# Optimization experiments

Hardware: AMD Instinct MI355X
Metric: run time of the kernel (lower is better)

## Reference

```python
import jax, jax.numpy as jnp
import numpy as np

B, N, D = 4, 2048, 256
EPS = 1e-5


def _clinear(Z, W, b):
    # complex linear: Z (B,2,N,din), W (2,dout,din), b (2,dout)
    Zr, Zi = Z[:, 0], Z[:, 1]
    Wr, Wi = W[0], W[1]
    outr = Zr @ Wr.T - Zi @ Wi.T + b[0]
    outi = Zr @ Wi.T + Zi @ Wr.T + b[1]
    return jnp.stack([outr, outi], axis=1)


def setup_inputs() -> dict:
    key = jax.random.key(0)
    ks = jax.random.split(key, 14)
    sc = 1.0 / np.sqrt(D).astype(np.float32)
    t = jnp.tile(jnp.arange(N + 1, dtype=jnp.float32)[None] * 0.01, (B, 1))
    return {
        'Z_q': jax.random.normal(ks[0], (B, 2, N, D), jnp.float32),
        'Z_k': jax.random.normal(ks[1], (B, 2, N, D), jnp.float32),
        'Z_v': jax.random.normal(ks[2], (B, 2, N, D), jnp.float32),
        't_measure_all': t,
        'W_q': jax.random.normal(ks[3], (2, D, D), jnp.float32) * sc,
        'b_q': jax.random.normal(ks[4], (2, D), jnp.float32) * 0.01,
        'W_k': jax.random.normal(ks[5], (2, D, D), jnp.float32) * sc,
        'b_k': jax.random.normal(ks[6], (2, D), jnp.float32) * 0.01,
        'W_v': jax.random.normal(ks[7], (2, D, D), jnp.float32) * sc,
        'b_v': jax.random.normal(ks[8], (2, D), jnp.float32) * 0.01,
        'W_p': jax.random.normal(ks[9], (2, D, D), jnp.float32) * sc,
        'b_p': jax.random.normal(ks[10], (2, D), jnp.float32) * 0.01,
        'lambda1': jax.random.normal(ks[11], (2, D // 2, 1), jnp.float32),
        'lambda_Omega_sqrt': jax.random.normal(ks[12], (1, D, 1), jnp.float32) * sc,
        'lambda_Gamma_sqrt': jax.random.normal(ks[13], (1, D, 1), jnp.float32) * sc,
        'tau': jnp.asarray(1.0, jnp.float32),
        'delta': jnp.asarray(0.0, jnp.float32),
        'lambda_C': jnp.ones((1, D, 1), jnp.float32),
    }


def reference(Z_q, Z_k, Z_v, t_measure_all, W_q, b_q, W_k, b_k, W_v, b_v,
              W_p, b_p, lambda1, lambda_Omega_sqrt, lambda_Gamma_sqrt,
              tau, delta, lambda_C):
    # lambda_h = 0 * compute_lambda_h(lambda1): conjugate-pair spectrum, zeroed in forward
    lam_r = 0.0 * jnp.concatenate([lambda1[0], lambda1[0]], axis=0)[:, 0]   # (D,)
    lam_i = 0.0 * jnp.concatenate([lambda1[1], -lambda1[1]], axis=0)[:, 0]  # (D,)
    lam_Om = lambda_Omega_sqrt ** 2 + EPS   # process noise (1,D,1)
    lam_Ga = lambda_Gamma_sqrt ** 2 + EPS   # measurement noise (1,D,1)

    Q = _clinear(Z_q, W_q, b_q)  # (B,2,N,D)
    K = _clinear(Z_k, W_k, b_k)
    V = _clinear(Z_v, W_v, b_v)

    t = t_measure_all[0, :-1]  # (N,)
    # exponential state-transition kernels exp(+/- lambda * t): (2,N,D)
    mag_f = jnp.exp(lam_r[None] * t[:, None]); ph_f = lam_i[None] * t[:, None]
    exp_f = jnp.stack([mag_f * jnp.cos(ph_f), mag_f * jnp.sin(ph_f)])
    mag_b = jnp.exp(-lam_r[None] * t[:, None]); ph_b = -lam_i[None] * t[:, None]
    exp_b = jnp.stack([mag_b * jnp.cos(ph_b), mag_b * jnp.sin(ph_b)])
    # one-step transition exp(lambda * dt): (2,D)
    dt = t[1] - t[0]
    mat_exp = jnp.stack([jnp.exp(lam_r * dt) * jnp.cos(lam_i * dt),
                         jnp.exp(lam_r * dt) * jnp.sin(lam_i * dt)])

    # averaged covariance kernel, exact lambda->0 limit: Gamma + Omega*|t_i-t_j|, mean over D
    lamC2 = lambda_C[0, :, 0] ** 2
    ga_bar = jnp.mean(lamC2 * lam_Ga[0, :, 0])
    om_bar = jnp.mean(lamC2 * lam_Om[0, :, 0])
    abs_dt = jnp.abs(t[:, None] - t[None, :])          # (N,N)
    V_avg_ij = ga_bar + om_bar * abs_dt                # (N,N)

    # factorized kernels
    V_v = exp_f[None]                 # (1,2,N,D)
    U_q = exp_b[None] * Q             # (B,2,N,D)
    U_k = exp_b[None] * K
    U_v = exp_b[None] * V

    # precision-weighted squared residual norm R_ij = sum_d |V_k|^2 |U_q_i - U_k_j|^2
    Vk_abs = jnp.sum(exp_f ** 2, axis=0)              # (N,D)
    Uk_abs = jnp.sum(U_k ** 2, axis=1)                # (B,N,D)
    Uq_abs = jnp.sum(U_q ** 2, axis=1)                # (B,N,D)
    T1 = jnp.einsum('id,bjd->bij', Vk_abs, Uk_abs)
    T2 = jnp.sum(Vk_abs[None] * Uq_abs, axis=2)[:, :, None]
    T3 = (jnp.einsum('bid,bjd->bij', Vk_abs[None] * U_q[:, 0], U_k[:, 0]) +
          jnp.einsum('bid,bjd->bij', Vk_abs[None] * U_q[:, 1], U_k[:, 1]))
    R_qk_abs = T1 + T2 - 2.0 * T3                     # (B,N,N)

    scores = -(tau ** 2) * jnp.log(V_avg_ij[None] + R_qk_abs)
    mask = jnp.tril(jnp.ones((N, N), bool))
    scores = jnp.where(mask[None], scores, -jnp.inf)
    A = jax.nn.softmax(scores, axis=2)                # (B,N,N)
    Q_ij = jnp.stack([A, jnp.zeros_like(A)], axis=1)  # (B,2,N,N)

    # est_inner = complex matmul(Q_ij, U_v); Q imag part is zero
    est_inner = jnp.stack([jnp.einsum('bij,bjd->bid', A, U_v[:, 0]),
                           jnp.einsum('bij,bjd->bid', A, U_v[:, 1])], axis=1)
    est_v = V_v * est_inner          # plain elementwise product, as in source
    s = jax.nn.sigmoid(delta)
    est_eigenbasis = (1.0 - s) * V + s * est_v        # (B,2,N,D)

    # complex Hadamard with one-step transition
    pr = mat_exp[0][None, None] * est_eigenbasis[:, 0] - mat_exp[1][None, None] * est_eigenbasis[:, 1]
    pi = mat_exp[0][None, None] * est_eigenbasis[:, 1] + mat_exp[1][None, None] * est_eigenbasis[:, 0]
    pred_p = jnp.stack([pr, pi], axis=1)
    out = _clinear(pred_p, W_p, b_p)                  # (B,2,N,D)

    lambda_h = jnp.stack([lam_r, lam_i])[..., None]
    return est_eigenbasis, out, Q_ij, V_v, U_v, lambda_h
```

## Files before the change

### kernel.cpp

```cpp
#include <hip/hip_runtime.h>
#include <math.h>

#define BN 4
#define NN 2048
#define DD 256
#define EPSF 1e-5f

typedef __attribute__((ext_vector_type(8))) short bf16x8;
typedef __attribute__((ext_vector_type(4))) float f32x4;

constexpr size_t OFF_EST = 0;
constexpr size_t OFF_OUT = (size_t)BN * 2 * NN * DD;
constexpr size_t OFF_QIJ = OFF_OUT + (size_t)BN * 2 * NN * DD;
constexpr size_t OFF_VV  = OFF_QIJ + (size_t)BN * 2 * NN * NN;
constexpr size_t OFF_UV  = OFF_VV + (size_t)2 * NN * DD;
constexpr size_t OFF_LH  = OFF_UV + (size_t)BN * 2 * NN * DD;

constexpr size_t SCR_B0   = OFF_QIJ + (size_t)NN * NN;
constexpr size_t U_Q16    = 0;
constexpr size_t U_K16    = (size_t)BN * NN * DD;
constexpr size_t U_VT16   = 2 * (size_t)BN * NN * DD;
constexpr size_t SCR_QN   = SCR_B0 + 3 * (size_t)BN * NN * DD / 2;
constexpr size_t SCR_KN   = SCR_QN + (size_t)BN * NN;
constexpr size_t SCR_L    = SCR_KN + (size_t)BN * NN;
constexpr size_t SCR_SC   = SCR_L + (size_t)BN * NN;
constexpr size_t SCR_W16P = SCR_SC + 16;
constexpr size_t SCR_E16F = OFF_QIJ + 3 * (size_t)NN * NN;
constexpr size_t U_PART   = (size_t)BN * NN * 512;
constexpr size_t SCR_Z16F = OFF_QIJ + 5 * (size_t)NN * NN;
constexpr size_t SCR_Z16VF = OFF_QIJ + 7 * (size_t)NN * NN;
constexpr size_t U_W16    = (size_t)BN * NN * 512;

constexpr size_t W16_PER_B = 136 * 16384;

__device__ __forceinline__ short f2bf(float x) {
    union { float f; unsigned u; } v; v.f = x;
    unsigned r = v.u + 0x7fff + ((v.u >> 16) & 1);
    return (short)(r >> 16);
}
__device__ __forceinline__ float bf2f(unsigned short h) {
    union { unsigned u; float f; } v; v.u = ((unsigned)h) << 16;
    return v.f;
}
__device__ __forceinline__ unsigned short* u16p(float* d, size_t fofs) {
    return (unsigned short*)(d + fofs);
}
__device__ __forceinline__ const unsigned short* u16pc(const float* d, size_t fofs) {
    return (const unsigned short*)(d + fofs);
}
__device__ __forceinline__ unsigned short* w16p(float* d, int b) {
    return (b < 3) ? u16p(d, SCR_Z16F) + (size_t)b * W16_PER_B
                   : u16p(d, SCR_Z16VF);
}
__device__ __forceinline__ const unsigned short* w16pc(const float* d, int b) {
    return (b < 3) ? u16pc(d, SCR_Z16F) + (size_t)b * W16_PER_B
                   : u16pc(d, SCR_Z16VF);
}
__device__ __forceinline__ int nc_of(int TI) { return TI >= 12 ? 3 : (TI >= 6 ? 2 : 1); }
__device__ __forceinline__ int cb_of(int TI) {
    return TI < 6 ? TI : (TI < 12 ? 6 + 2 * (TI - 6) : 18 + 3 * (TI - 12));
}

__device__ __forceinline__ void gll16(const unsigned short* g, short* l) {
    __builtin_amdgcn_global_load_lds(
        (const __attribute__((address_space(1))) unsigned*)g,
        (__attribute__((address_space(3))) unsigned*)l, 16, 0, 0);
}
__device__ __forceinline__ void stage_tile(const unsigned short* gbase, size_t stride_sh,
                                           short* ldsbuf, int t) {
    const int w = t >> 6, L = t & 63;
#pragma unroll
    for (int p = 0; p < 2; ++p) {
        const int r0 = w * 32 + p * 16;
        const unsigned short* src = gbase + (size_t)(r0 + (L >> 2)) * stride_sh + (L & 3) * 8;
        gll16(src, ldsbuf + r0 * 32);
    }
}

__global__ void k_cvt(const float* __restrict__ Zq, const float* __restrict__ Zk,
                      const float* __restrict__ Zv,
                      const float* __restrict__ Wq, const float* __restrict__ Wk,
                      const float* __restrict__ Wv, const float* __restrict__ Wp,
                      const float* __restrict__ tau, const float* __restrict__ delta,
                      const float* __restrict__ lamOm, const float* __restrict__ lamGa,
                      const float* __restrict__ lamC,
                      float* __restrict__ dout) {
    const int z = blockIdx.z;
    if (z < 3) {
        const float* Z = (z == 0) ? Zq : (z == 1) ? Zk : Zv;
        unsigned short* O = (z == 0) ? u16p(dout, SCR_Z16F)
                          : (z == 1) ? u16p(dout, SCR_Z16F) + (size_t)BN * NN * 512
                                     : u16p(dout, SCR_Z16VF);
        const long n4 = (long)BN * 2 * NN * DD / 4;
        for (long i4 = (long)blockIdx.x * 256 + threadIdx.x; i4 < n4;
             i4 += (long)gridDim.x * 256) {
            const long i = i4 * 4;
            const int d = (int)(i & (DD - 1));
            const long r = i >> 8;
            const int n = (int)(r & (NN - 1));
            const long bc = r >> 11;
            const int c = (int)(bc & 1), b = (int)(bc >> 1);
            float4 v = *(const float4*)&Z[i];
            ushort4 o;
            o.x = (unsigned short)f2bf(v.x); o.y = (unsigned short)f2bf(v.y);
            o.z = (unsigned short)f2bf(v.z); o.w = (unsigned short)f2bf(v.w);
            *(ushort4*)&O[((size_t)(b * NN + n)) * 512 + c * 256 + d] = o;
        }
    } else if (z == 3) {
        const float* Ws[4] = {Wq, Wk, Wv, Wp};
        const long n4 = 6L * 256 * 512 / 4;
        for (long e4 = (long)blockIdx.x * 256 + threadIdx.x; e4 < n4;
             e4 += (long)gridDim.x * 256) {
            const long e = e4 * 4;
            const int k = (int)(e & 511);
            const long rest = e >> 9;
            const int dd = (int)(rest & 255);
            const int m = (int)(rest >> 8);
            int proj, mode;
            if (m < 3)      { proj = m; mode = 0; }
            else if (m == 3){ proj = 2; mode = 1; }
            else            { proj = 3; mode = m - 4; }
            const int kc = k >> 8, kk = k & 255;
            int wc; float sgn;
            if (mode == 0) { wc = kc; sgn = kc ? -1.f : 1.f; }
            else           { wc = 1 - kc; sgn = 1.f; }
            float4 v = *(const float4*)&Ws[proj][((size_t)wc * DD + dd) * DD + kk];
            ushort4 o;
            o.x = (unsigned short)f2bf(sgn * v.x); o.y = (unsigned short)f2bf(sgn * v.y);
            o.z = (unsigned short)f2bf(sgn * v.z); o.w = (unsigned short)f2bf(sgn * v.w);
            unsigned short* dst = (m < 4)
                ? u16p(dout, SCR_Z16VF) + U_W16 + (size_t)m * 131072
                : u16p(dout, SCR_W16P) + (size_t)(m - 4) * 131072;
            *(ushort4*)&dst[(size_t)dd * 512 + k] = o;
        }
    } else {
        const int idx = blockIdx.x * 256 + threadIdx.x;
        if (idx < 3 * BN * NN) dout[SCR_QN + idx] = 0.f;
        if (blockIdx.x == 0) {
            __shared__ float red[8];
            const int t = threadIdx.x;
            float c2 = lamC[t] * lamC[t];
            float ga = c2 * (lamGa[t] * lamGa[t] + EPSF);
            float om = c2 * (lamOm[t] * lamOm[t] + EPSF);
            for (int o = 32; o > 0; o >>= 1) {
                ga += __shfl_down(ga, o, 64);
                om += __shfl_down(om, o, 64);
            }
            if ((t & 63) == 0) { red[t >> 6] = ga; red[4 + (t >> 6)] = om; }
            __syncthreads();
            if (t == 0) {
                float gs = red[0] + red[1] + red[2] + red[3];
                float os = red[4] + red[5] + red[6] + red[7];
                float* scal = dout + SCR_SC;
                scal[0] = tau[0] * tau[0];
                scal[1] = 1.f / (1.f + __expf(-delta[0]));
                scal[2] = gs / 256.f;
                scal[3] = os / 256.f;
            }
        }
    }
}

__global__ __launch_bounds__(256) void k_qkv(const float* __restrict__ bq,
                                             const float* __restrict__ bk,
                                             const float* __restrict__ bv,
                                             float* __restrict__ dout)
{
    __shared__ short Al[128 * 32];
    __shared__ short Bl[128 * 32];
    const int z = blockIdx.z;
    const int d0 = blockIdx.x * 128;
    const int b = blockIdx.y >> 4;
    const int n0 = (blockIdx.y & 15) * 128;

    const unsigned short* Z16 =
        (z == 0) ? u16pc(dout, SCR_Z16F)
      : (z == 1) ? u16pc(dout, SCR_Z16F) + (size_t)BN * NN * 512
                 : u16pc(dout, SCR_Z16VF);
    const unsigned short* W16 = u16pc(dout, SCR_Z16VF) + U_W16 + (size_t)z * 131072;
    const float* bias = (z == 0) ? bq : (z == 1) ? bk : bv;
    const int bofs = (z == 3) ? DD : 0;

    const int t = threadIdx.x, wave = t >> 6, lane = t & 63, quad = lane >> 4, lm = lane & 15;
    const int wm = (wave >> 1) * 64, wn = (wave & 1) * 64;
    const unsigned short* Abase = Z16 + (size_t)(b * NN + n0) * 512;
    const unsigned short* Bbase = W16 + (size_t)d0 * 512;

    f32x4 acc[4][4];
#pragma unroll
    for (int i = 0; i < 4; ++i)
#pragma unroll
        for (int j = 0; j < 4; ++j) acc[i][j] = (f32x4){0.f, 0.f, 0.f, 0.f};

    for (int kt = 0; kt < 16; ++kt) {
        const int kk0 = kt * 32;
        stage_tile(Abase + kk0, 512, Al, t);
        stage_tile(Bbase + kk0, 512, Bl, t);
        __syncthreads();
        bf16x8 af[4], bff[4];
#pragma unroll
        for (int mi = 0; mi < 4; ++mi) af[mi] = *(const bf16x8*)&Al[(wm + mi * 16 + lm) * 32 + quad * 8];
#pragma unroll
        for (int nj = 0; nj < 4; ++nj) bff[nj] = *(const bf16x8*)&Bl[(wn + nj * 16 + lm) * 32 + quad * 8];
#pragma unroll
        for (int mi = 0; mi < 4; ++mi)
#pragma unroll
            for (int nj = 0; nj < 4; ++nj)
                acc[mi][nj] = __builtin_amdgcn_mfma_f32_16x16x32_bf16(af[mi], bff[nj], acc[mi][nj], 0, 0, 0);
        __syncthreads();
    }

    if (z <= 1) {
        unsigned short* O16 = u16p(dout, SCR_B0) + (z ? U_K16 : U_Q16) + (size_t)b * NN * DD;
        float* NRM = dout + (z ? SCR_KN : SCR_QN) + b * NN;
#pragma unroll
        for (int mi = 0; mi < 4; ++mi)
#pragma unroll
            for (int r = 0; r < 4; ++r) {
                const int m = n0 + wm + mi * 16 + quad * 4 + r;
                float ss = 0.f;
#pragma unroll
                for (int nj = 0; nj < 4; ++nj) {
                    const int d = d0 + wn + nj * 16 + lm;
                    unsigned short h = (unsigned short)f2bf(acc[mi][nj][r] + bias[d]);
                    O16[(size_t)m * DD + d] = h;
                    const float vb = bf2f(h);
                    ss = fmaf(vb, vb, ss);
                }
                ss += __shfl_down(ss, 8, 16); ss += __shfl_down(ss, 4, 16);
                ss += __shfl_down(ss, 2, 16); ss += __shfl_down(ss, 1, 16);
                if (lm == 0) atomicAdd(&NRM[m], ss);
            }
    } else if (z == 2) {
        float* UV0 = dout + OFF_UV + (size_t)(b * 2) * NN * DD;
#pragma unroll
        for (int mi = 0; mi < 4; ++mi)
#pragma unroll
            for (int r = 0; r < 4; ++r) {
                const int m = n0 + wm + mi * 16 + quad * 4 + r;
#pragma unroll
                for (int nj = 0; nj < 4; ++nj) {
                    const int d = d0 + wn + nj * 16 + lm;
                    UV0[(size_t)m * DD + d] = acc[mi][nj][r] + bias[d];
                }
            }
    } else {
        const float s1 = 1.f - dout[SCR_SC + 1];
        float* EST1 = dout + OFF_EST + (size_t)(b * 2 + 1) * NN * DD;
        unsigned short* E16 = u16p(dout, SCR_E16F) + (size_t)b * NN * 512;
#pragma unroll
        for (int mi = 0; mi < 4; ++mi)
#pragma unroll
            for (int r = 0; r < 4; ++r) {
                const int m = n0 + wm + mi * 16 + quad * 4 + r;
#pragma unroll
                for (int nj = 0; nj < 4; ++nj) {
                    const int d = d0 + wn + nj * 16 + lm;
                    const float v = s1 * (acc[mi][nj][r] + bias[bofs + d]);
                    EST1[(size_t)m * DD + d] = v;
                    E16[(size_t)m * 512 + 256 + d] = (unsigned short)f2bf(v);
                }
            }
    }
}

__global__ __launch_bounds__(256) void k_outproj(const float* __restrict__ bp,
                                                 float* __restrict__ dout)
{
    __shared__ short Al[128 * 32];
    __shared__ short Bl[128 * 32];
    const int z = blockIdx.z;
    const int d0 = blockIdx.x * 128;
    const int b = blockIdx.y >> 4;
    const int n0 = (blockIdx.y & 15) * 128;
    const unsigned short* E16 = u16pc(dout, SCR_E16F) + (size_t)b * NN * 512;
    const unsigned short* W16 = u16pc(dout, SCR_W16P) + (size_t)z * 131072;

    const int t = threadIdx.x, wave = t >> 6, lane = t & 63, quad = lane >> 4, lm = lane & 15;
    const int wm = (wave >> 1) * 64, wn = (wave & 1) * 64;
    const unsigned short* Abase = E16 + (size_t)n0 * 512;
    const unsigned short* Bbase = W16 + (size_t)d0 * 512;

    f32x4 acc[4][4];
#pragma unroll
    for (int i = 0; i < 4; ++i)
#pragma unroll
        for (int j = 0; j < 4; ++j) acc[i][j] = (f32x4){0.f, 0.f, 0.f, 0.f};

    for (int kt = 0; kt < 16; ++kt) {
        const int kk0 = kt * 32;
        stage_tile(Abase + kk0, 512, Al, t);
        stage_tile(Bbase + kk0, 512, Bl, t);
        __syncthreads();
        bf16x8 af[4], bff[4];
#pragma unroll
        for (int mi = 0; mi < 4; ++mi) af[mi] = *(const bf16x8*)&Al[(wm + mi * 16 + lm) * 32 + quad * 8];
#pragma unroll
        for (int nj = 0; nj < 4; ++nj) bff[nj] = *(const bf16x8*)&Bl[(wn + nj * 16 + lm) * 32 + quad * 8];
#pragma unroll
        for (int mi = 0; mi < 4; ++mi)
#pragma unroll
            for (int nj = 0; nj < 4; ++nj)
                acc[mi][nj] = __builtin_amdgcn_mfma_f32_16x16x32_bf16(af[mi], bff[nj], acc[mi][nj], 0, 0, 0);
        __syncthreads();
    }
    const int bofs = z ? DD : 0;
    float* O = dout + OFF_OUT + (size_t)(b * 2 + z) * NN * DD;
#pragma unroll
    for (int mi = 0; mi < 4; ++mi)
#pragma unroll
        for (int r = 0; r < 4; ++r) {
            const int m = n0 + wm + mi * 16 + quad * 4 + r;
#pragma unroll
            for (int nj = 0; nj < 4; ++nj) {
                const int d = d0 + wn + nj * 16 + lm;
                O[(size_t)m * DD + d] = acc[mi][nj][r] + bp[bofs + d];
            }
        }
}

__global__ void k_vtrans(float* __restrict__ dout) {
    __shared__ float T[64][65];
    const int b = blockIdx.z;
    const int nb = blockIdx.x * 64, db = blockIdx.y * 64;
    const float* V = dout + OFF_UV + (size_t)(b * 2) * NN * DD;
    unsigned short* VT = u16p(dout, SCR_B0) + U_VT16 + (size_t)b * DD * NN;
    const int tr = threadIdx.x >> 4, tc = (threadIdx.x & 15) * 4;
#pragma unroll
    for (int p = 0; p < 4; ++p) {
        float4 v = *(const float4*)&V[(size_t)(nb + tr + p * 16) * DD + db + tc];
        T[tr + p * 16][tc + 0] = v.x; T[tr + p * 16][tc + 1] = v.y;
        T[tr + p * 16][tc + 2] = v.z; T[tr + p * 16][tc + 3] = v.w;
    }
    __syncthreads();
#pragma unroll
    for (int p = 0; p < 4; ++p) {
        const int d = tr + p * 16;
        ushort4 o;
        o.x = (unsigned short)f2bf(T[tc + 0][d]);
        o.y = (unsigned short)f2bf(T[tc + 1][d]);
        o.z = (unsigned short)f2bf(T[tc + 2][d]);
        o.w = (unsigned short)f2bf(T[tc + 3][d]);
        *(ushort4*)&VT[(size_t)(db + d) * NN + nb + tc] = o;
    }
}

__global__ __launch_bounds__(256) void k_scores(const float* __restrict__ tmeas,
                                                float* __restrict__ dout) {
    __shared__ short Al[128 * 32];
    __shared__ short Bl[128 * 32];
    const int b = blockIdx.y, x = blockIdx.x;
    int ti = (int)((sqrtf(8.f * x + 1.f) - 1.f) * 0.5f);
    while ((ti + 1) * (ti + 2) / 2 <= x) ++ti;
    while (ti * (ti + 1) / 2 > x) --ti;
    const int tj = x - ti * (ti + 1) / 2;
    const int i0 = ti * 128, j0 = tj * 128;
    const unsigned short* Q16 = u16pc(dout, SCR_B0) + U_Q16 + (size_t)b * NN * DD;
    const unsigned short* K16 = u16pc(dout, SCR_B0) + U_K16 + (size_t)b * NN * DD;
    const int t = threadIdx.x, wave = t >> 6, lane = t & 63, quad = lane >> 4, lm = lane & 15;
    const int wm = (wave >> 1) * 64, wn = (wave & 1) * 64;
    const unsigned short* Abase = Q16 + (size_t)i0 * DD;
    const unsigned short* Bbase = K16 + (size_t)j0 * DD;

    f32x4 acc[4][4];
#pragma unroll
    for (int i = 0; i < 4; ++i)
#pragma unroll
        for (int j = 0; j < 4; ++j) acc[i][j] = (f32x4){0.f, 0.f, 0.f, 0.f};

    for (int kt = 0; kt < 8; ++kt) {
        const int kk0 = kt * 32;
        stage_tile(Abase + kk0, DD, Al, t);
        stage_tile(Bbase + kk0, DD, Bl, t);
        __syncthreads();
        bf16x8 af[4], bff[4];
#pragma unroll
        for (int mi = 0; mi < 4; ++mi) af[mi] = *(const bf16x8*)&Al[(wm + mi * 16 + lm) * 32 + quad * 8];
#pragma unroll
        for (int nj = 0; nj < 4; ++nj) bff[nj] = *(const bf16x8*)&Bl[(wn + nj * 16 + lm) * 32 + quad * 8];
#pragma unroll
        for (int mi = 0; mi < 4; ++mi)
#pragma unroll
            for (int nj = 0; nj < 4; ++nj)
                acc[mi][nj] = __builtin_amdgcn_mfma_f32_16x16x32_bf16(af[mi], bff[nj], acc[mi][nj], 0, 0, 0);
        __syncthreads();
    }

    const float tau2 = dout[SCR_SC + 0], ga = dout[SCR_SC + 2], om = dout[SCR_SC + 3];
    unsigned short* WT = w16p(dout, b) + (size_t)x * 16384;
    const float* QN_ = dout + SCR_QN + b * NN;
    const float* KN_ = dout + SCR_KN + b * NN;
    float kn[4], tjv[4]; int jj[4];
#pragma unroll
    for (int nj = 0; nj < 4; ++nj) {
        jj[nj] = j0 + wn + nj * 16 + lm;
        kn[nj] = KN_[jj[nj]];
        tjv[nj] = tmeas[jj[nj]];
    }
#pragma unroll
    for (int mi = 0; mi < 4; ++mi)
#pragma unroll
        for (int r = 0; r < 4; ++r) {
            const int li = wm + mi * 16 + quad * 4 + r;
            const int i = i0 + li;
            const float qni = QN_[i], tqi = tmeas[i];
            float rs = 0.f;
#pragma unroll
            for (int nj = 0; nj < 4; ++nj) {
                float xx = ga + om * fabsf(tqi - tjv[nj]) + qni + kn[nj] - 2.f * acc[mi][nj][r];
                xx = fmaxf(xx, 1e-30f);
                float w = (tau2 == 1.f) ? __builtin_amdgcn_rcpf(xx)
                                        : __expf(-tau2 * __logf(xx));
                if (jj[nj] > i) w = 0.f;
                const unsigned short h = (unsigned short)f2bf(w);
                WT[(size_t)li * 128 + (wn + nj * 16 + lm)] = h;
                rs += bf2f(h);
            }
            rs += __shfl_down(rs, 8, 16); rs += __shfl_down(rs, 4, 16);
            rs += __shfl_down(rs, 2, 16); rs += __shfl_down(rs, 1, 16);
            if (lm == 0) atomicAdd(&dout[SCR_L + b * NN + i], rs);
        }
}

__global__ __launch_bounds__(256) void k_estinner(float* __restrict__ dout) {
    __shared__ short Al[128 * 32];
    __shared__ short Bl[128 * 32];
    const int b = blockIdx.y;
    const int chunk = blockIdx.x >> 1, half = blockIdx.x & 1;
    int y = chunk, TI = 0, cb = 0;
    for (;;) { const int nc = nc_of(TI); if (y < nc) break; y -= nc; cb += nc; ++TI; }
    const int kbeg = y * 768;
    const int kend = min(kbeg + 768, (TI + 1) * 128);
    const int nst = (kend - kbeg) >> 5;
    const int cidx = cb + y;
    const int tri = TI * (TI + 1) / 2;
    const unsigned short* WT = w16pc(dout, b);
    const unsigned short* VT = u16pc(dout, SCR_B0) + U_VT16 + (size_t)b * DD * NN
                             + (size_t)(half * 128) * NN;

    const int t = threadIdx.x, wave = t >> 6, lane = t & 63, quad = lane >> 4, lm = lane & 15;
    const int wm = (wave >> 1) * 64, wn = (wave & 1) * 64;

    f32x4 acc[4][4];
#pragma unroll
    for (int i = 0; i < 4; ++i)
#pragma unroll
        for (int j = 0; j < 4; ++j) acc[i][j] = (f32x4){0.f, 0.f, 0.f, 0.f};

    for (int kt = 0; kt < nst; ++kt) {
        const int kk0 = kbeg + kt * 32;
        const int tile = kk0 >> 7;
        stage_tile(WT + (size_t)(tri + tile) * 16384 + (kk0 & 127), 128, Al, t);
        stage_tile(VT + kk0, NN, Bl, t);
        __syncthreads();
        bf16x8 af[4], bff[4];
#pragma unroll
        for (int mi = 0; mi < 4; ++mi) af[mi] = *(const bf16x8*)&Al[(wm + mi * 16 + lm) * 32 + quad * 8];
#pragma unroll
        for (int nj = 0; nj < 4; ++nj) bff[nj] = *(const bf16x8*)&Bl[(wn + nj * 16 + lm) * 32 + quad * 8];
#pragma unroll
        for (int mi = 0; mi < 4; ++mi)
#pragma unroll
            for (int nj = 0; nj < 4; ++nj)
                acc[mi][nj] = __builtin_amdgcn_mfma_f32_16x16x32_bf16(af[mi], bff[nj], acc[mi][nj], 0, 0, 0);
        __syncthreads();
    }
    unsigned short* P = u16p(dout, SCR_E16F) + U_PART +
                        ((size_t)(b * 30 + cidx)) * 128 * 256;
#pragma unroll
    for (int mi = 0; mi < 4; ++mi)
#pragma unroll
        for (int r = 0; r < 4; ++r) {
            const int ri = wm + mi * 16 + quad * 4 + r;
#pragma unroll
            for (int nj = 0; nj < 4; ++nj) {
                const int d = half * 128 + wn + nj * 16 + lm;
                P[(size_t)ri * 256 + d] = (unsigned short)f2bf(acc[mi][nj][r]);
            }
        }
}

__global__ void k_blendfills(float* __restrict__ dout) {
    const int z = blockIdx.z;
    if (z < 4) {
        const int b = z;
        if (blockIdx.x >= 512) return;
        const int t = threadIdx.x;
        const int i = blockIdx.x * 4 + (t >> 6);
        const int d4 = (t & 63) * 4;
        const int TI = i >> 7;
        const int nc = nc_of(TI), cb = cb_of(TI);
        const float s = dout[SCR_SC + 1];
        const float linv = 1.f / dout[SCR_L + b * NN + i];
        const unsigned short* P = u16pc(dout, SCR_E16F) + U_PART;
        float4 sum = {0.f, 0.f, 0.f, 0.f};
        for (int c = 0; c < nc; ++c) {
            ushort4 pv = *(const ushort4*)&P[((size_t)(b * 30 + cb + c) * 128 + (i & 127)) * 256 + d4];
            sum.x += bf2f(pv.x); sum.y += bf2f(pv.y);
            sum.z += bf2f(pv.z); sum.w += bf2f(pv.w);
        }
        const float4 vr = *(const float4*)&dout[OFF_UV + ((size_t)(b * 2) * NN + i) * DD + d4];
        const float sl = s * linv;
        float4 ev;
        ev.x = (1.f - s) * vr.x + sl * sum.x;
        ev.y = (1.f - s) * vr.y + sl * sum.y;
        ev.z = (1.f - s) * vr.z + sl * sum.z;
        ev.w = (1.f - s) * vr.w + sl * sum.w;
        *(float4*)&dout[OFF_EST + ((size_t)(b * 2) * NN + i) * DD + d4] = ev;
        ushort4 o;
        o.x = (unsigned short)f2bf(ev.x); o.y = (unsigned short)f2bf(ev.y);
        o.z = (unsigned short)f2bf(ev.z); o.w = (unsigned short)f2bf(ev.w);
        *(ushort4*)&u16p(dout, SCR_E16F)[((size_t)(b * NN + i)) * 512 + d4] = o;
        return;
    }
    if (z < 8) {
        const int b = z - 4, i = blockIdx.x;
        const int TI = i >> 7, li = i & 127;
        const int tri = TI * (TI + 1) / 2;
        const float linv = 1.f / dout[SCR_L + b * NN + i];
        const unsigned short* WTb = w16pc(dout, b);
        float* row = dout + OFF_QIJ + (size_t)b * 2 * NN * NN + (size_t)i * NN;
        for (int j4 = threadIdx.x * 4; j4 < NN; j4 += 1024) {
            const int tj = j4 >> 7;
            float4 o = {0.f, 0.f, 0.f, 0.f};
            if (tj <= TI) {
                ushort4 h = *(const ushort4*)&WTb[((size_t)(tri + tj)) * 16384
                                                  + (size_t)li * 128 + (j4 & 127)];
                o.x = bf2f(h.x) * linv; o.y = bf2f(h.y) * linv;
                o.z = bf2f(h.z) * linv; o.w = bf2f(h.w) * linv;
            }
            *(float4*)&row[j4] = o;
        }
        return;
    }
    size_t base; long n; float val = 0.f;
    if (z == 8)       { base = SCR_B0; n = 3145728; }
    else if (z == 9)  { base = OFF_VV; n = (long)NN * DD; val = 1.f; }
    else if (z == 10) { base = OFF_VV + (size_t)NN * DD; n = (long)NN * DD; }
    else if (z < 15)  { base = OFF_UV + (size_t)(2 * (z - 11) + 1) * NN * DD; n = (long)NN * DD; }
    else              { base = OFF_LH; n = 512; }
    float* p = dout + base;
    const float4 v = {val, val, val, val};
    for (long i = ((long)blockIdx.x * 256 + threadIdx.x) * 4; i < n;
         i += (long)gridDim.x * 1024)
        *(float4*)&p[i] = v;
}

extern "C" void kernel_launch(void* const* d_in, const int* in_sizes, int n_in,
                              void* d_out, int out_size, void* d_ws, size_t ws_size,
                              hipStream_t stream) {
    const float* Zq = (const float*)d_in[0];
    const float* Zk = (const float*)d_in[1];
    const float* Zv = (const float*)d_in[2];
    const float* tm = (const float*)d_in[3];
    const float* Wq = (const float*)d_in[4];
    const float* bq = (const float*)d_in[5];
    const float* Wk = (const float*)d_in[6];
    const float* bk = (const float*)d_in[7];
    const float* Wv = (const float*)d_in[8];
    const float* bv = (const float*)d_in[9];
    const float* Wp = (const float*)d_in[10];
    const float* bp = (const float*)d_in[11];
    const float* lamOm = (const float*)d_in[13];
    const float* lamGa = (const float*)d_in[14];
    const float* tau = (const float*)d_in[15];
    const float* delta = (const float*)d_in[16];
    const float* lamC = (const float*)d_in[17];
    float* out = (float*)d_out;

    k_cvt<<<dim3(2048, 1, 5), dim3(256), 0, stream>>>(
        Zq, Zk, Zv, Wq, Wk, Wv, Wp, tau, delta, lamOm, lamGa, lamC, out);
    k_qkv<<<dim3(2, 64, 4), dim3(256), 0, stream>>>(bq, bk, bv, out);
    k_vtrans<<<dim3(32, 4, 4), dim3(256), 0, stream>>>(out);
    k_scores<<<dim3(136, 4), dim3(256), 0, stream>>>(tm, out);
    k_estinner<<<dim3(60, 4), dim3(256), 0, stream>>>(out);
    k_blendfills<<<dim3(2048, 1, 16), dim3(256), 0, stream>>>(out);
    k_outproj<<<dim3(2, 64, 2), dim3(256), 0, stream>>>(bp, out);
    hipMemsetAsync((void*)(out + SCR_Z16F),  0, (size_t)NN * NN * 4, stream);
    hipMemsetAsync((void*)(out + SCR_Z16VF), 0, (size_t)NN * NN * 4, stream);
    hipMemsetAsync((void*)(out + SCR_E16F),  0, (size_t)NN * NN * 4, stream);
    hipMemsetAsync((void*)(out + SCR_QN),    0, ((size_t)NN * NN - 3145728) * 4, stream);
}
```

Baseline: 352.2 us.

## Fuse all stages into one persistent kernel with software grid barriers

Replaces seven separate kernel launches with a single persistent kernel of 512 blocks that runs each stage in turn, separated by an atomic-counter grid barrier. The fill work from the old blend kernel moves into the first stage. The aim is to remove per-launch overhead and the tail idle time between dependent kernels. The cost is spin-wait barriers, and correctness depends on all 512 blocks being co-resident; launch_bounds(256,2) is set for that.

New measurement: 1.120 ms. 3.18x slower.

```diff
diff --git a/kernel.cpp b/kernel.cpp
--- a/kernel.cpp
+++ b/kernel.cpp
@@ -30,8 +30,9 @@
 constexpr size_t SCR_Z16F = OFF_QIJ + 5 * (size_t)NN * NN;
 constexpr size_t SCR_Z16VF = OFF_QIJ + 7 * (size_t)NN * NN;
 constexpr size_t U_W16    = (size_t)BN * NN * 512;
-
 constexpr size_t W16_PER_B = 136 * 16384;
+
+#define NBLK 512
 
 __device__ __forceinline__ short f2bf(float x) {
     union { float f; unsigned u; } v; v.f = x;
@@ -61,6 +62,26 @@
     return TI < 6 ? TI : (TI < 12 ? 6 + 2 * (TI - 6) : 18 + 3 * (TI - 12));
 }
 
+__device__ __forceinline__ void gbar(float* dout) {
+    __syncthreads();
+    if (threadIdx.x == 0) {
+        unsigned* cnt = (unsigned*)(dout + SCR_SC + 8);
+        unsigned* gen = cnt + 1;
+        __threadfence();
+        unsigned g = __hip_atomic_load(gen, __ATOMIC_RELAXED, __HIP_MEMORY_SCOPE_AGENT);
+        unsigned a = __hip_atomic_fetch_add(cnt, 1u, __ATOMIC_ACQ_REL, __HIP_MEMORY_SCOPE_AGENT);
+        if (a == (unsigned)NBLK - 1) {
+            __hip_atomic_store(cnt, 0u, __ATOMIC_RELAXED, __HIP_MEMORY_SCOPE_AGENT);
+            __hip_atomic_fetch_add(gen, 1u, __ATOMIC_RELEASE, __HIP_MEMORY_SCOPE_AGENT);
+        } else {
+            while (__hip_atomic_load(gen, __ATOMIC_ACQUIRE, __HIP_MEMORY_SCOPE_AGENT) == g)
+                __builtin_amdgcn_s_sleep(2);
+        }
+        __threadfence();
+    }
+    __syncthreads();
+}
+
 __device__ __forceinline__ void gll16(const unsigned short* g, short* l) {
     __builtin_amdgcn_global_load_lds(
         (const __attribute__((address_space(1))) unsigned*)g,
@@ -77,23 +98,35 @@
     }
 }
 
-__global__ void k_cvt(const float* __restrict__ Zq, const float* __restrict__ Zk,
-                      const float* __restrict__ Zv,
-                      const float* __restrict__ Wq, const float* __restrict__ Wk,
-                      const float* __restrict__ Wv, const float* __restrict__ Wp,
-                      const float* __restrict__ tau, const float* __restrict__ delta,
-                      const float* __restrict__ lamOm, const float* __restrict__ lamGa,
-                      const float* __restrict__ lamC,
-                      float* __restrict__ dout) {
-    const int z = blockIdx.z;
-    if (z < 3) {
-        const float* Z = (z == 0) ? Zq : (z == 1) ? Zk : Zv;
-        unsigned short* O = (z == 0) ? u16p(dout, SCR_Z16F)
-                          : (z == 1) ? u16p(dout, SCR_Z16F) + (size_t)BN * NN * 512
-                                     : u16p(dout, SCR_Z16VF);
-        const long n4 = (long)BN * 2 * NN * DD / 4;
-        for (long i4 = (long)blockIdx.x * 256 + threadIdx.x; i4 < n4;
-             i4 += (long)gridDim.x * 256) {
+__global__ __launch_bounds__(256, 2) void k_mega(
+    const float* __restrict__ Zq, const float* __restrict__ Zk,
+    const float* __restrict__ Zv, const float* __restrict__ tmeas,
+    const float* __restrict__ Wq, const float* __restrict__ bq,
+    const float* __restrict__ Wk, const float* __restrict__ bk,
+    const float* __restrict__ Wv, const float* __restrict__ bv,
+    const float* __restrict__ Wp, const float* __restrict__ bp,
+    const float* __restrict__ lamOm, const float* __restrict__ lamGa,
+    const float* __restrict__ tau, const float* __restrict__ delta,
+    const float* __restrict__ lamC, float* __restrict__ dout)
+{
+    __shared__ __align__(16) float smemf[4160];
+    short* Al = (short*)smemf;
+    short* Bl = ((short*)smemf) + 4096;
+
+    const int t = threadIdx.x;
+    const int wave = t >> 6, lane = t & 63, quad = lane >> 4, lm = lane & 15;
+    const int wm = (wave >> 1) * 64, wn = (wave & 1) * 64;
+
+    {
+        const long tid = (long)blockIdx.x * 256 + t;
+        const long nthr = (long)gridDim.x * 256;
+        for (long u = tid; u < 3L * 1048576; u += nthr) {
+            const int zz = (int)(u >> 20);
+            const long i4 = u & 1048575;
+            const float* Z = (zz == 0) ? Zq : (zz == 1) ? Zk : Zv;
+            unsigned short* O = (zz == 0) ? u16p(dout, SCR_Z16F)
+                              : (zz == 1) ? u16p(dout, SCR_Z16F) + (size_t)BN * NN * 512
+                                          : u16p(dout, SCR_Z16VF);
             const long i = i4 * 4;
             const int d = (int)(i & (DD - 1));
             const long r = i >> 8;
@@ -106,25 +139,22 @@
             o.z = (unsigned short)f2bf(v.z); o.w = (unsigned short)f2bf(v.w);
             *(ushort4*)&O[((size_t)(b * NN + n)) * 512 + c * 256 + d] = o;
         }
-    } else if (z == 3) {
-        const float* Ws[4] = {Wq, Wk, Wv, Wp};
-        const long n4 = 6L * 256 * 512 / 4;
-        for (long e4 = (long)blockIdx.x * 256 + threadIdx.x; e4 < n4;
-             e4 += (long)gridDim.x * 256) {
+        for (long e4 = tid; e4 < 196608; e4 += nthr) {
             const long e = e4 * 4;
             const int k = (int)(e & 511);
             const long rest = e >> 9;
             const int dd = (int)(rest & 255);
             const int m = (int)(rest >> 8);
-            int proj, mode;
-            if (m < 3)      { proj = m; mode = 0; }
-            else if (m == 3){ proj = 2; mode = 1; }
-            else            { proj = 3; mode = m - 4; }
+            const float* Ws = (m == 0) ? Wq : (m == 1) ? Wk : (m <= 3) ? Wv : Wp;
+            int mode;
+            if (m < 3)      { mode = 0; }
+            else if (m == 3){ mode = 1; }
+            else            { mode = m - 4; }
             const int kc = k >> 8, kk = k & 255;
             int wc; float sgn;
             if (mode == 0) { wc = kc; sgn = kc ? -1.f : 1.f; }
             else           { wc = 1 - kc; sgn = 1.f; }
-            float4 v = *(const float4*)&Ws[proj][((size_t)wc * DD + dd) * DD + kk];
+            float4 v = *(const float4*)&Ws[((size_t)wc * DD + dd) * DD + kk];
             ushort4 o;
             o.x = (unsigned short)f2bf(sgn * v.x); o.y = (unsigned short)f2bf(sgn * v.y);
             o.z = (unsigned short)f2bf(sgn * v.z); o.w = (unsigned short)f2bf(sgn * v.w);
@@ -133,12 +163,21 @@
                 : u16p(dout, SCR_W16P) + (size_t)(m - 4) * 131072;
             *(ushort4*)&dst[(size_t)dd * 512 + k] = o;
         }
-    } else {
-        const int idx = blockIdx.x * 256 + threadIdx.x;
-        if (idx < 3 * BN * NN) dout[SCR_QN + idx] = 0.f;
+        const float4 ones = {1.f, 1.f, 1.f, 1.f};
+        const float4 zz4 = {0.f, 0.f, 0.f, 0.f};
+        float* VV0 = dout + OFF_VV;
+        for (long u = tid; u < 131072; u += nthr) *(float4*)&VV0[u * 4] = ones;
+        float* VV1 = dout + OFF_VV + (size_t)NN * DD;
+        for (long u = tid; u < 131072; u += nthr) *(float4*)&VV1[u * 4] = zz4;
+        for (int b = 0; b < BN; ++b) {
+            float* U1 = dout + OFF_UV + (size_t)(2 * b + 1) * NN * DD;
+            for (long u = tid; u < 131072; u += nthr) *(float4*)&U1[u * 4] = zz4;
+        }
+        float* LH = dout + OFF_LH;
+        for (long u = tid; u < 128; u += nthr) *(float4*)&LH[u * 4] = zz4;
+        for (long u = tid; u < 6144; u += nthr) *(float4*)&dout[SCR_QN + u * 4] = zz4;
         if (blockIdx.x == 0) {
-            __shared__ float red[8];
-            const int t = threadIdx.x;
+            float* red = smemf;
             float c2 = lamC[t] * lamC[t];
             float ga = c2 * (lamGa[t] * lamGa[t] + EPSF);
             float om = c2 * (lamOm[t] * lamOm[t] + EPSF);
@@ -159,391 +198,365 @@
             }
         }
     }
-}
-
-__global__ __launch_bounds__(256) void k_qkv(const float* __restrict__ bq,
-                                             const float* __restrict__ bk,
-                                             const float* __restrict__ bv,
-                                             float* __restrict__ dout)
-{
-    __shared__ short Al[128 * 32];
-    __shared__ short Bl[128 * 32];
-    const int z = blockIdx.z;
-    const int d0 = blockIdx.x * 128;
-    const int b = blockIdx.y >> 4;
-    const int n0 = (blockIdx.y & 15) * 128;
-
-    const unsigned short* Z16 =
-        (z == 0) ? u16pc(dout, SCR_Z16F)
-      : (z == 1) ? u16pc(dout, SCR_Z16F) + (size_t)BN * NN * 512
-                 : u16pc(dout, SCR_Z16VF);
-    const unsigned short* W16 = u16pc(dout, SCR_Z16VF) + U_W16 + (size_t)z * 131072;
-    const float* bias = (z == 0) ? bq : (z == 1) ? bk : bv;
-    const int bofs = (z == 3) ? DD : 0;
-
-    const int t = threadIdx.x, wave = t >> 6, lane = t & 63, quad = lane >> 4, lm = lane & 15;
-    const int wm = (wave >> 1) * 64, wn = (wave & 1) * 64;
-    const unsigned short* Abase = Z16 + (size_t)(b * NN + n0) * 512;
-    const unsigned short* Bbase = W16 + (size_t)d0 * 512;
-
-    f32x4 acc[4][4];
-#pragma unroll
-    for (int i = 0; i < 4; ++i)
-#pragma unroll
-        for (int j = 0; j < 4; ++j) acc[i][j] = (f32x4){0.f, 0.f, 0.f, 0.f};
-
-    for (int kt = 0; kt < 16; ++kt) {
-        const int kk0 = kt * 32;
-        stage_tile(Abase + kk0, 512, Al, t);
-        stage_tile(Bbase + kk0, 512, Bl, t);
+    gbar(dout);
+
+    {
+        const int job = blockIdx.x;
+        const int z = job >> 7;
+        const int rem = job & 127;
+        const int d0 = (rem & 1) * 128;
+        const int by = rem >> 1;
+        const int b = by >> 4;
+        const int n0 = (by & 15) * 128;
+
+        const unsigned short* Z16 =
+            (z == 0) ? u16pc(dout, SCR_Z16F)
+          : (z == 1) ? u16pc(dout, SCR_Z16F) + (size_t)BN * NN * 512
+                     : u16pc(dout, SCR_Z16VF);
+        const unsigned short* W16 = u16pc(dout, SCR_Z16VF) + U_W16 + (size_t)z * 131072;
+        const float* bias = (z == 0) ? bq : (z == 1) ? bk : bv;
+        const int bofs = (z == 3) ? DD : 0;
+        const unsigned short* Abase = Z16 + (size_t)(b * NN + n0) * 512;
+        const unsigned short* Bbase = W16 + (size_t)d0 * 512;
+
+        f32x4 acc[4][4];
+#pragma unroll
+        for (int i = 0; i < 4; ++i)
+#pragma unroll
+            for (int j = 0; j < 4; ++j) acc[i][j] = (f32x4){0.f, 0.f, 0.f, 0.f};
+
+        for (int kt = 0; kt < 16; ++kt) {
+            const int kk0 = kt * 32;
+            stage_tile(Abase + kk0, 512, Al, t);
+            stage_tile(Bbase + kk0, 512, Bl, t);
+            __syncthreads();
+            bf16x8 af[4], bff[4];
+#pragma unroll
+            for (int mi = 0; mi < 4; ++mi) af[mi] = *(const bf16x8*)&Al[(wm + mi * 16 + lm) * 32 + quad * 8];
+#pragma unroll
+            for (int nj = 0; nj < 4; ++nj) bff[nj] = *(const bf16x8*)&Bl[(wn + nj * 16 + lm) * 32 + quad * 8];
+#pragma unroll
+            for (int mi = 0; mi < 4; ++mi)
+#pragma unroll
+                for (int nj = 0; nj < 4; ++nj)
+                    acc[mi][nj] = __builtin_amdgcn_mfma_f32_16x16x32_bf16(af[mi], bff[nj], acc[mi][nj], 0, 0, 0);
+            __syncthreads();
+        }
+
+        if (z <= 1) {
+            unsigned short* O16 = u16p(dout, SCR_B0) + (z ? U_K16 : U_Q16) + (size_t)b * NN * DD;
+            float* NRM = dout + (z ? SCR_KN : SCR_QN) + b * NN;
+#pragma unroll
+            for (int mi = 0; mi < 4; ++mi)
+#pragma unroll
+                for (int r = 0; r < 4; ++r) {
+                    const int m = n0 + wm + mi * 16 + quad * 4 + r;
+                    float ss = 0.f;
+#pragma unroll
+                    for (int nj = 0; nj < 4; ++nj) {
+                        const int d = d0 + wn + nj * 16 + lm;
+                        unsigned short h = (unsigned short)f2bf(acc[mi][nj][r] + bias[d]);
+                        O16[(size_t)m * DD + d] = h;
+                        const float vb = bf2f(h);
+                        ss = fmaf(vb, vb, ss);
+                    }
+                    ss += __shfl_down(ss, 8, 16); ss += __shfl_down(ss, 4, 16);
+                    ss += __shfl_down(ss, 2, 16); ss += __shfl_down(ss, 1, 16);
+                    if (lm == 0) atomicAdd(&NRM[m], ss);
+                }
+        } else if (z == 2) {
+            float* UV0 = dout + OFF_UV + (size_t)(b * 2) * NN * DD;
+#pragma unroll
+            for (int mi = 0; mi < 4; ++mi)
+#pragma unroll
+                for (int r = 0; r < 4; ++r) {
+                    const int m = n0 + wm + mi * 16 + quad * 4 + r;
+#pragma unroll
+                    for (int nj = 0; nj < 4; ++nj) {
+                        const int d = d0 + wn + nj * 16 + lm;
+                        UV0[(size_t)m * DD + d] = acc[mi][nj][r] + bias[d];
+                    }
+                }
+        } else {
+            const float s1 = 1.f - dout[SCR_SC + 1];
+            float* EST1 = dout + OFF_EST + (size_t)(b * 2 + 1) * NN * DD;
+            unsigned short* E16 = u16p(dout, SCR_E16F) + (size_t)b * NN * 512;
+#pragma unroll
+            for (int mi = 0; mi < 4; ++mi)
+#pragma unroll
+                for (int r = 0; r < 4; ++r) {
+                    const int m = n0 + wm + mi * 16 + quad * 4 + r;
+#pragma unroll
+                    for (int nj = 0; nj < 4; ++nj) {
+                        const int d = d0 + wn + nj * 16 + lm;
+                        const float v = s1 * (acc[mi][nj][r] + bias[bofs + d]);
+                        EST1[(size_t)m * DD + d] = v;
+                        E16[(size_t)m * 512 + 256 + d] = (unsigned short)f2bf(v);
+                    }
+                }
+        }
+    }
+    gbar(dout);
+
+    {
+        float (*T)[65] = (float(*)[65])smemf;
+        const int job = blockIdx.x;
+        const int b = job >> 7, rem = job & 127;
+        const int db = (rem >> 5) * 64, nb = (rem & 31) * 64;
+        const float* V = dout + OFF_UV + (size_t)(b * 2) * NN * DD;
+        unsigned short* VT = u16p(dout, SCR_B0) + U_VT16 + (size_t)b * DD * NN;
+        const int tr = t >> 4, tc = (t & 15) * 4;
+#pragma unroll
+        for (int p = 0; p < 4; ++p) {
+            float4 v = *(const float4*)&V[(size_t)(nb + tr + p * 16) * DD + db + tc];
+            T[tr + p * 16][tc + 0] = v.x; T[tr + p * 16][tc + 1] = v.y;
+            T[tr + p * 16][tc + 2] = v.z; T[tr + p * 16][tc + 3] = v.w;
+        }
         __syncthreads();
-        bf16x8 af[4], bff[4];
-#pragma unroll
-        for (int mi = 0; mi < 4; ++mi) af[mi] = *(const bf16x8*)&Al[(wm + mi * 16 + lm) * 32 + quad * 8];
-#pragma unroll
-        for (int nj = 0; nj < 4; ++nj) bff[nj] = *(const bf16x8*)&Bl[(wn + nj * 16 + lm) * 32 + quad * 8];
+#pragma unroll
+        for (int p = 0; p < 4; ++p) {
+            const int d = tr + p * 16;
+            ushort4 o;
+            o.x = (unsigned short)f2bf(T[tc + 0][d]);
+            o.y = (unsigned short)f2bf(T[tc + 1][d]);
+            o.z = (unsigned short)f2bf(T[tc + 2][d]);
+            o.w = (unsigned short)f2bf(T[tc + 3][d]);
+            *(ushort4*)&VT[(size_t)(db + d) * NN + nb + tc] = o;
+        }
+        __syncthreads();
+    }
+    gbar(dout);
+
+    for (int xj = blockIdx.x; xj < 544; xj += gridDim.x) {
+        const int b = xj / 136, x = xj % 136;
+        int ti = (int)((sqrtf(8.f * x + 1.f) - 1.f) * 0.5f);
+        while ((ti + 1) * (ti + 2) / 2 <= x) ++ti;
+        while (ti * (ti + 1) / 2 > x) --ti;
+        const int tj = x - ti * (ti + 1) / 2;
+        const int i0 = ti * 128, j0 = tj * 128;
+        const unsigned short* Q16 = u16pc(dout, SCR_B0) + U_Q16 + (size_t)b * NN * DD;
+        const unsigned short* K16 = u16pc(dout, SCR_B0) + U_K16 + (size_t)b * NN * DD;
+        const unsigned short* Abase = Q16 + (size_t)i0 * DD;
+        const unsigned short* Bbase = K16 + (size_t)j0 * DD;
+
+        f32x4 acc[4][4];
+#pragma unroll
+        for (int i = 0; i < 4; ++i)
+#pragma unroll
+            for (int j = 0; j < 4; ++j) acc[i][j] = (f32x4){0.f, 0.f, 0.f, 0.f};
+
+        for (int kt = 0; kt < 8; ++kt) {
+            const int kk0 = kt * 32;
+            stage_tile(Abase + kk0, DD, Al, t);
+            stage_tile(Bbase + kk0, DD, Bl, t);
+            __syncthreads();
+            bf16x8 af[4], bff[4];
+#pragma unroll
+            for (int mi = 0; mi < 4; ++mi) af[mi] = *(const bf16x8*)&Al[(wm + mi * 16 + lm) * 32 + quad * 8];
+#pragma unroll
+            for (int nj = 0; nj < 4; ++nj) bff[nj] = *(const bf16x8*)&Bl[(wn + nj * 16 + lm) * 32 + quad * 8];
+#pragma unroll
+            for (int mi = 0; mi < 4; ++mi)
+#pragma unroll
+                for (int nj = 0; nj < 4; ++nj)
+                    acc[mi][nj] = __builtin_amdgcn_mfma_f32_16x16x32_bf16(af[mi], bff[nj], acc[mi][nj], 0, 0, 0);
+            __syncthreads();
+        }
+
+        const float tau2 = dout[SCR_SC + 0], ga = dout[SCR_SC + 2], om = dout[SCR_SC + 3];
+        unsigned short* WT = w16p(dout, b) + (size_t)x * 16384;
+        const float* QN_ = dout + SCR_QN + b * NN;
+        const float* KN_ = dout + SCR_KN + b * NN;
+        float kn[4], tjv[4]; int jj[4];
+#pragma unroll
+        for (int nj = 0; nj < 4; ++nj) {
+            jj[nj] = j0 + wn + nj * 16 + lm;
+            kn[nj] = KN_[jj[nj]];
+            tjv[nj] = tmeas[jj[nj]];
+        }
 #pragma unroll
         for (int mi = 0; mi < 4; ++mi)
 #pragma unroll
-            for (int nj = 0; nj < 4; ++nj)
-                acc[mi][nj] = __builtin_amdgcn_mfma_f32_16x16x32_bf16(af[mi], bff[nj], acc[mi][nj], 0, 0, 0);
-        __syncthreads();
-    }
-
-    if (z <= 1) {
-        unsigned short* O16 = u16p(dout, SCR_B0) + (z ? U_K16 : U_Q16) + (size_t)b * NN * DD;
-        float* NRM = dout + (z ? SCR_KN : SCR_QN) + b * NN;
+            for (int r = 0; r < 4; ++r) {
+                const int li = wm + mi * 16 + quad * 4 + r;
+                const int i = i0 + li;
+                const float qni = QN_[i], tqi = tmeas[i];
+                float rs = 0.f;
+#pragma unroll
+                for (int nj = 0; nj < 4; ++nj) {
+                    float xx = ga + om * fabsf(tqi - tjv[nj]) + qni + kn[nj] - 2.f * acc[mi][nj][r];
+                    xx = fmaxf(xx, 1e-30f);
+                    float w = (tau2 == 1.f) ? __builtin_amdgcn_rcpf(xx)
+                                            : __expf(-tau2 * __logf(xx));
+                    if (jj[nj] > i) w = 0.f;
+                    const unsigned short h = (unsigned short)f2bf(w);
+                    WT[(size_t)li * 128 + (wn + nj * 16 + lm)] = h;
+                    rs += bf2f(h);
+                }
+                rs += __shfl_down(rs, 8, 16); rs += __shfl_down(rs, 4, 16);
+                rs += __shfl_down(rs, 2, 16); rs += __shfl_down(rs, 1, 16);
+                if (lm == 0) atomicAdd(&dout[SCR_L + b * NN + i], rs);
+            }
+    }
+    gbar(dout);
+
+    for (int job = blockIdx.x; job < 240; job += gridDim.x) {
+        const int b = job / 60, xx = job % 60;
+        const int chunk = xx >> 1, half = xx & 1;
+        int y = chunk, TI = 0, cb = 0;
+        for (;;) { const int nc = nc_of(TI); if (y < nc) break; y -= nc; cb += nc; ++TI; }
+        const int kbeg = y * 768;
+        const int kend = min(kbeg + 768, (TI + 1) * 128);
+        const int nst = (kend - kbeg) >> 5;
+        const int cidx = cb + y;
+        const int tri = TI * (TI + 1) / 2;
+        const unsigned short* WT = w16pc(dout, b);
+        const unsigned short* VT = u16pc(dout, SCR_B0) + U_VT16 + (size_t)b * DD * NN
+                                 + (size_t)(half * 128) * NN;
+
+        f32x4 acc[4][4];
+#pragma unroll
+        for (int i = 0; i < 4; ++i)
+#pragma unroll
+            for (int j = 0; j < 4; ++j) acc[i][j] = (f32x4){0.f, 0.f, 0.f, 0.f};
+
+        for (int kt = 0; kt < nst; ++kt) {
+            const int kk0 = kbeg + kt * 32;
+            const int tile = kk0 >> 7;
+            stage_tile(WT + (size_t)(tri + tile) * 16384 + (kk0 & 127), 128, Al, t);
+            stage_tile(VT + kk0, NN, Bl, t);
+            __syncthreads();
+            bf16x8 af[4], bff[4];
+#pragma unroll
+            for (int mi = 0; mi < 4; ++mi) af[mi] = *(const bf16x8*)&Al[(wm + mi * 16 + lm) * 32 + quad * 8];
+#pragma unroll
+            for (int nj = 0; nj < 4; ++nj) bff[nj] = *(const bf16x8*)&Bl[(wn + nj * 16 + lm) * 32 + quad * 8];
+#pragma unroll
+            for (int mi = 0; mi < 4; ++mi)
+#pragma unroll
+                for (int nj = 0; nj < 4; ++nj)
+                    acc[mi][nj] = __builtin_amdgcn_mfma_f32_16x16x32_bf16(af[mi], bff[nj], acc[mi][nj], 0, 0, 0);
+            __syncthreads();
+        }
+        unsigned short* P = u16p(dout, SCR_E16F) + U_PART +
+                            ((size_t)(b * 30 + cidx)) * 128 * 256;
 #pragma unroll
         for (int mi = 0; mi < 4; ++mi)
 #pragma unroll
             for (int r = 0; r < 4; ++r) {
-                const int m = n0 + wm + mi * 16 + quad * 4 + r;
-                float ss = 0.f;
+                const int ri = wm + mi * 16 + quad * 4 + r;
 #pragma unroll
                 for (int nj = 0; nj < 4; ++nj) {
-                    const int d = d0 + wn + nj * 16 + lm;
-                    unsigned short h = (unsigned short)f2bf(acc[mi][nj][r] + bias[d]);
-                    O16[(size_t)m * DD + d] = h;
-                    const float vb = bf2f(h);
-                    ss = fmaf(vb, vb, ss);
-                }
-                ss += __shfl_down(ss, 8, 16); ss += __shfl_down(ss, 4, 16);
-                ss += __shfl_down(ss, 2, 16); ss += __shfl_down(ss, 1, 16);
-                if (lm == 0) atomicAdd(&NRM[m], ss);
-            }
-    } else if (z == 2) {
-        float* UV0 = dout + OFF_UV + (size_t)(b * 2) * NN * DD;
-#pragma unroll
-        for (int mi = 0; mi < 4; ++mi)
-#pragma unroll
-            for (int r = 0; r < 4; ++r) {
-                const int m = n0 + wm + mi * 16 + quad * 4 + r;
-#pragma unroll
-                for (int nj = 0; nj < 4; ++nj) {
-                    const int d = d0 + wn + nj * 16 + lm;
-                    UV0[(size_t)m * DD + d] = acc[mi][nj][r] + bias[d];
-                }
-            }
-    } else {
-        const float s1 = 1.f - dout[SCR_SC + 1];
-        float* EST1 = dout + OFF_EST + (size_t)(b * 2 + 1) * NN * DD;
-        unsigned short* E16 = u16p(dout, SCR_E16F) + (size_t)b * NN * 512;
-#pragma unroll
-        for (int mi = 0; mi < 4; ++mi)
-#pragma unroll
-            for (int r = 0; r < 4; ++r) {
-                const int m = n0 + wm + mi * 16 + quad * 4 + r;
-#pragma unroll
-                for (int nj = 0; nj < 4; ++nj) {
-                    const int d = d0 + wn + nj * 16 + lm;
-                    const float v = s1 * (acc[mi][nj][r] + bias[bofs + d]);
-                    EST1[(size_t)m * DD + d] = v;
-                    E16[(size_t)m * 512 + 256 + d] = (unsigned short)f2bf(v);
-                }
-            }
-    }
-}
-
-__global__ __launch_bounds__(256) void k_outproj(const float* __restrict__ bp,
-                                                 float* __restrict__ dout)
-{
-    __shared__ short Al[128 * 32];
-    __shared__ short Bl[128 * 32];
-    const int z = blockIdx.z;
-    const int d0 = blockIdx.x * 128;
-    const int b = blockIdx.y >> 4;
-    const int n0 = (blockIdx.y & 15) * 128;
-    const unsigned short* E16 = u16pc(dout, SCR_E16F) + (size_t)b * NN * 512;
-    const unsigned short* W16 = u16pc(dout, SCR_W16P) + (size_t)z * 131072;
-
-    const int t = threadIdx.x, wave = t >> 6, lane = t & 63, quad = lane >> 4, lm = lane & 15;
-    const int wm = (wave >> 1) * 64, wn = (wave & 1) * 64;
-    const unsigned short* Abase = E16 + (size_t)n0 * 512;
-    const unsigned short* Bbase = W16 + (size_t)d0 * 512;
-
-    f32x4 acc[4][4];
-#pragma unroll
-    for (int i = 0; i < 4; ++i)
-#pragma unroll
-        for (int j = 0; j < 4; ++j) acc[i][j] = (f32x4){0.f, 0.f, 0.f, 0.f};
-
-    for (int kt = 0; kt < 16; ++kt) {
-        const int kk0 = kt * 32;
-        stage_tile(Abase + kk0, 512, Al, t);
-        stage_tile(Bbase + kk0, 512, Bl, t);
-        __syncthreads();
-        bf16x8 af[4], bff[4];
-#pragma unroll
-        for (int mi = 0; mi < 4; ++mi) af[mi] = *(const bf16x8*)&Al[(wm + mi * 16 + lm) * 32 + quad * 8];
-#pragma unroll
-        for (int nj = 0; nj < 4; ++nj) bff[nj] = *(const bf16x8*)&Bl[(wn + nj * 16 + lm) * 32 + quad * 8];
-#pragma unroll
-        for (int mi = 0; mi < 4; ++mi)
-#pragma unroll
-            for (int nj = 0; nj < 4; ++nj)
-                acc[mi][nj] = __builtin_amdgcn_mfma_f32_16x16x32_bf16(af[mi], bff[nj], acc[mi][nj], 0, 0, 0);
-        __syncthreads();
-    }
-    const int bofs = z ? DD : 0;
-    float* O = dout + OFF_OUT + (size_t)(b * 2 + z) * NN * DD;
-#pragma unroll
-    for (int mi = 0; mi < 4; ++mi)
-#pragma unroll
-        for (int r = 0; r < 4; ++r) {
-            const int m = n0 + wm + mi * 16 + quad * 4 + r;
-#pragma unroll
-            for (int nj = 0; nj < 4; ++nj) {
-                const int d = d0 + wn + nj * 16 + lm;
-                O[(size_t)m * DD + d] = acc[mi][nj][r] + bp[bofs + d];
-            }
-        }
-}
-
-__global__ void k_vtrans(float* __restrict__ dout) {
-    __shared__ float T[64][65];
-    const int b = blockIdx.z;
-    const int nb = blockIdx.x * 64, db = blockIdx.y * 64;
-    const float* V = dout + OFF_UV + (size_t)(b * 2) * NN * DD;
-    unsigned short* VT = u16p(dout, SCR_B0) + U_VT16 + (size_t)b * DD * NN;
-    const int tr = threadIdx.x >> 4, tc = (threadIdx.x & 15) * 4;
-#pragma unroll
-    for (int p = 0; p < 4; ++p) {
-        float4 v = *(const float4*)&V[(size_t)(nb + tr + p * 16) * DD + db + tc];
-        T[tr + p * 16][tc + 0] = v.x; T[tr + p * 16][tc + 1] = v.y;
-        T[tr + p * 16][tc + 2] = v.z; T[tr + p * 16][tc + 3] = v.w;
-    }
-    __syncthreads();
-#pragma unroll
-    for (int p = 0; p < 4; ++p) {
-        const int d = tr + p * 16;
-        ushort4 o;
-        o.x = (unsigned short)f2bf(T[tc + 0][d]);
-        o.y = (unsigned short)f2bf(T[tc + 1][d]);
-        o.z = (unsigned short)f2bf(T[tc + 2][d]);
-        o.w = (unsigned short)f2bf(T[tc + 3][d]);
-        *(ushort4*)&VT[(size_t)(db + d) * NN + nb + tc] = o;
-    }
-}
-
-__global__ __launch_bounds__(256) void k_scores(const float* __restrict__ tmeas,
-                                                float* __restrict__ dout) {
-    __shared__ short Al[128 * 32];
-    __shared__ short Bl[128 * 32];
-    const int b = blockIdx.y, x = blockIdx.x;
-    int ti = (int)((sqrtf(8.f * x + 1.f) - 1.f) * 0.5f);
-    while ((ti + 1) * (ti + 2) / 2 <= x) ++ti;
-    while (ti * (ti + 1) / 2 > x) --ti;
-    const int tj = x - ti * (ti + 1) / 2;
-    const int i0 = ti * 128, j0 = tj * 128;
-    const unsigned short* Q16 = u16pc(dout, SCR_B0) + U_Q16 + (size_t)b * NN * DD;
-    const unsigned short* K16 = u16pc(dout, SCR_B0) + U_K16 + (size_t)b * NN * DD;
-    const int t = threadIdx.x, wave = t >> 6, lane = t & 63, quad = lane >> 4, lm = lane & 15;
-    const int wm = (wave >> 1) * 64, wn = (wave & 1) * 64;
-    const unsigned short* Abase = Q16 + (size_t)i0 * DD;
-    const unsigned short* Bbase = K16 + (size_t)j0 * DD;
-
-    f32x4 acc[4][4];
-#pragma unroll
-    for (int i = 0; i < 4; ++i)
-#pragma unroll
-        for (int j = 0; j < 4; ++j) acc[i][j] = (f32x4){0.f, 0.f, 0.f, 0.f};
-
-    for (int kt = 0; kt < 8; ++kt) {
-        const int kk0 = kt * 32;
-        stage_tile(Abase + kk0, DD, Al, t);
-        stage_tile(Bbase + kk0, DD, Bl, t);
-        __syncthreads();
-        bf16x8 af[4], bff[4];
-#pragma unroll
-        for (int mi = 0; mi < 4; ++mi) af[mi] = *(const bf16x8*)&Al[(wm + mi * 16 + lm) * 32 + quad * 8];
-#pragma unroll
-        for (int nj = 0; nj < 4; ++nj) bff[nj] = *(const bf16x8*)&Bl[(wn + nj * 16 + lm) * 32 + quad * 8];
-#pragma unroll
-        for (int mi = 0; mi < 4; ++mi)
-#pragma unroll
-            for (int nj = 0; nj < 4; ++nj)
-                acc[mi][nj] = __builtin_amdgcn_mfma_f32_16x16x32_bf16(af[mi], bff[nj], acc[mi][nj], 0, 0, 0);
-        __syncthreads();
-    }
-
-    const float tau2 = dout[SCR_SC + 0], ga = dout[SCR_SC + 2], om = dout[SCR_SC + 3];
-    unsigned short* WT = w16p(dout, b) + (size_t)x * 16384;
-    const float* QN_ = dout + SCR_QN + b * NN;
-    const float* KN_ = dout + SCR_KN + b * NN;
-    float kn[4], tjv[4]; int jj[4];
-#pragma unroll
-    for (int nj = 0; nj < 4; ++nj) {
-        jj[nj] = j0 + wn + nj * 16 + lm;
-        kn[nj] = KN_[jj[nj]];
-        tjv[nj] = tmeas[jj[nj]];
-    }
-#pragma unroll
-    for (int mi = 0; mi < 4; ++mi)
-#pragma unroll
-        for (int r = 0; r < 4; ++r) {
-            const int li = wm + mi * 16 + quad * 4 + r;
-            const int i = i0 + li;
-            const float qni = QN_[i], tqi = tmeas[i];
-            float rs = 0.f;
-#pragma unroll
-            for (int nj = 0; nj < 4; ++nj) {
-                float xx = ga + om * fabsf(tqi - tjv[nj]) + qni + kn[nj] - 2.f * acc[mi][nj][r];
-                xx = fmaxf(xx, 1e-30f);
-                float w = (tau2 == 1.f) ? __builtin_amdgcn_rcpf(xx)
-                                        : __expf(-tau2 * __logf(xx));
-                if (jj[nj] > i) w = 0.f;
-                const unsigned short h = (unsigned short)f2bf(w);
-                WT[(size_t)li * 128 + (wn + nj * 16 + lm)] = h;
-                rs += bf2f(h);
-            }
-            rs += __shfl_down(rs, 8, 16); rs += __shfl_down(rs, 4, 16);
-            rs += __shfl_down(rs, 2, 16); rs += __shfl_down(rs, 1, 16);
-            if (lm == 0) atomicAdd(&dout[SCR_L + b * NN + i], rs);
-        }
-}
-
-__global__ __launch_bounds__(256) void k_estinner(float* __restrict__ dout) {
-    __shared__ short Al[128 * 32];
-    __shared__ short Bl[128 * 32];
-    const int b = blockIdx.y;
-    const int chunk = blockIdx.x >> 1, half = blockIdx.x & 1;
-    int y = chunk, TI = 0, cb = 0;
-    for (;;) { const int nc = nc_of(TI); if (y < nc) break; y -= nc; cb += nc; ++TI; }
-    const int kbeg = y * 768;
-    const int kend = min(kbeg + 768, (TI + 1) * 128);
-    const int nst = (kend - kbeg) >> 5;
-    const int cidx = cb + y;
-    const int tri = TI * (TI + 1) / 2;
-    const unsigned short* WT = w16pc(dout, b);
-    const unsigned short* VT = u16pc(dout, SCR_B0) + U_VT16 + (size_t)b * DD * NN
-                             + (size_t)(half * 128) * NN;
-
-    const int t = threadIdx.x, wave = t >> 6, lane = t & 63, quad = lane >> 4, lm = lane & 15;
-    const int wm = (wave >> 1) * 64, wn = (wave & 1) * 64;
-
-    f32x4 acc[4][4];
-#pragma unroll
-    for (int i = 0; i < 4; ++i)
-#pragma unroll
-        for (int j = 0; j < 4; ++j) acc[i][j] = (f32x4){0.f, 0.f, 0.f, 0.f};
-
-    for (int kt = 0; kt < nst; ++kt) {
-        const int kk0 = kbeg + kt * 32;
-        const int tile = kk0 >> 7;
-        stage_tile(WT + (size_t)(tri + tile) * 16384 + (kk0 & 127), 128, Al, t);
-        stage_tile(VT + kk0, NN, Bl, t);
-        __syncthreads();
-        bf16x8 af[4], bff[4];
-#pragma unroll
-        for (int mi = 0; mi < 4; ++mi) af[mi] = *(const bf16x8*)&Al[(wm + mi * 16 + lm) * 32 + quad * 8];
-#pragma unroll
-        for (int nj = 0; nj < 4; ++nj) bff[nj] = *(const bf16x8*)&Bl[(wn + nj * 16 + lm) * 32 + quad * 8];
-#pragma unroll
-        for (int mi = 0; mi < 4; ++mi)
-#pragma unroll
-            for (int nj = 0; nj < 4; ++nj)
-                acc[mi][nj] = __builtin_amdgcn_mfma_f32_16x16x32_bf16(af[mi], bff[nj], acc[mi][nj], 0, 0, 0);
-        __syncthreads();
-    }
-    unsigned short* P = u16p(dout, SCR_E16F) + U_PART +
-                        ((size_t)(b * 30 + cidx)) * 128 * 256;
-#pragma unroll
-    for (int mi = 0; mi < 4; ++mi)
-#pragma unroll
-        for (int r = 0; r < 4; ++r) {
-            const int ri = wm + mi * 16 + quad * 4 + r;
-#pragma unroll
-            for (int nj = 0; nj < 4; ++nj) {
-                const int d = half * 128 + wn + nj * 16 + lm;
-                P[(size_t)ri * 256 + d] = (unsigned short)f2bf(acc[mi][nj][r]);
-            }
-        }
-}
-
-__global__ void k_blendfills(float* __restrict__ dout) {
-    const int z = blockIdx.z;
-    if (z < 4) {
-        const int b = z;
-        if (blockIdx.x >= 512) return;
-        const int t = threadIdx.x;
-        const int i = blockIdx.x * 4 + (t >> 6);
-        const int d4 = (t & 63) * 4;
-        const int TI = i >> 7;
-        const int nc = nc_of(TI), cb = cb_of(TI);
-        const float s = dout[SCR_SC + 1];
-        const float linv = 1.f / dout[SCR_L + b * NN + i];
-        const unsigned short* P = u16pc(dout, SCR_E16F) + U_PART;
-        float4 sum = {0.f, 0.f, 0.f, 0.f};
-        for (int c = 0; c < nc; ++c) {
-            ushort4 pv = *(const ushort4*)&P[((size_t)(b * 30 + cb + c) * 128 + (i & 127)) * 256 + d4];
-            sum.x += bf2f(pv.x); sum.y += bf2f(pv.y);
-            sum.z += bf2f(pv.z); sum.w += bf2f(pv.w);
-        }
-        const float4 vr = *(const float4*)&dout[OFF_UV + ((size_t)(b * 2) * NN + i) * DD + d4];
-        const float sl = s * linv;
-        float4 ev;
-        ev.x = (1.f - s) * vr.x + sl * sum.x;
-        ev.y = (1.f - s) * vr.y + sl * sum.y;
-        ev.z = (1.f - s) * vr.z + sl * sum.z;
-        ev.w = (1.f - s) * vr.w + sl * sum.w;
-        *(float4*)&dout[OFF_EST + ((size_t)(b * 2) * NN + i) * DD + d4] = ev;
-        ushort4 o;
-        o.x = (unsigned short)f2bf(ev.x); o.y = (unsigned short)f2bf(ev.y);
-        o.z = (unsigned short)f2bf(ev.z); o.w = (unsigned short)f2bf(ev.w);
-        *(ushort4*)&u16p(dout, SCR_E16F)[((size_t)(b * NN + i)) * 512 + d4] = o;
-        return;
-    }
-    if (z < 8) {
-        const int b = z - 4, i = blockIdx.x;
-        const int TI = i >> 7, li = i & 127;
-        const int tri = TI * (TI + 1) / 2;
-        const float linv = 1.f / dout[SCR_L + b * NN + i];
-        const unsigned short* WTb = w16pc(dout, b);
-        float* row = dout + OFF_QIJ + (size_t)b * 2 * NN * NN + (size_t)i * NN;
-        for (int j4 = threadIdx.x * 4; j4 < NN; j4 += 1024) {
-            const int tj = j4 >> 7;
-            float4 o = {0.f, 0.f, 0.f, 0.f};
-            if (tj <= TI) {
-                ushort4 h = *(const ushort4*)&WTb[((size_t)(tri + tj)) * 16384
-                                                  + (size_t)li * 128 + (j4 & 127)];
-                o.x = bf2f(h.x) * linv; o.y = bf2f(h.y) * linv;
-                o.z = bf2f(h.z) * linv; o.w = bf2f(h.w) * linv;
-            }
-            *(float4*)&row[j4] = o;
-        }
-        return;
-    }
-    size_t base; long n; float val = 0.f;
-    if (z == 8)       { base = SCR_B0; n = 3145728; }
-    else if (z == 9)  { base = OFF_VV; n = (long)NN * DD; val = 1.f; }
-    else if (z == 10) { base = OFF_VV + (size_t)NN * DD; n = (long)NN * DD; }
-    else if (z < 15)  { base = OFF_UV + (size_t)(2 * (z - 11) + 1) * NN * DD; n = (long)NN * DD; }
-    else              { base = OFF_LH; n = 512; }
-    float* p = dout + base;
-    const float4 v = {val, val, val, val};
-    for (long i = ((long)blockIdx.x * 256 + threadIdx.x) * 4; i < n;
-         i += (long)gridDim.x * 1024)
-        *(float4*)&p[i] = v;
+                    const int d = half * 128 + wn + nj * 16 + lm;
+                    P[(size_t)ri * 256 + d] = (unsigned short)f2bf(acc[mi][nj][r]);
+                }
+            }
+    }
+    gbar(dout);
+
+    for (int job = blockIdx.x; job < 10240; job += gridDim.x) {
+        if (job < 2048) {
+            const int b = job >> 9, x = job & 511;
+            const int i = x * 4 + (t >> 6);
+            const int d4 = (t & 63) * 4;
+            const int TI = i >> 7;
+            const int nc = nc_of(TI), cb = cb_of(TI);
+            const float s = dout[SCR_SC + 1];
+            const float linv = 1.f / dout[SCR_L + b * NN + i];
+            const unsigned short* P = u16pc(dout, SCR_E16F) + U_PART;
+            float4 sum = {0.f, 0.f, 0.f, 0.f};
+            for (int c = 0; c < nc; ++c) {
+                ushort4 pv = *(const ushort4*)&P[((size_t)(b * 30 + cb + c) * 128 + (i & 127)) * 256 + d4];
+                sum.x += bf2f(pv.x); sum.y += bf2f(pv.y);
+                sum.z += bf2f(pv.z); sum.w += bf2f(pv.w);
+            }
+            const float4 vr = *(const float4*)&dout[OFF_UV + ((size_t)(b * 2) * NN + i) * DD + d4];
+            const float sl = s * linv;
+            float4 ev;
+            ev.x = (1.f - s) * vr.x + sl * sum.x;
+            ev.y = (1.f - s) * vr.y + sl * sum.y;
+            ev.z = (1.f - s) * vr.z + sl * sum.z;
+            ev.w = (1.f - s) * vr.w + sl * sum.w;
+            *(float4*)&dout[OFF_EST + ((size_t)(b * 2) * NN + i) * DD + d4] = ev;
+            ushort4 o;
+            o.x = (unsigned short)f2bf(ev.x); o.y = (unsigned short)f2bf(ev.y);
+            o.z = (unsigned short)f2bf(ev.z); o.w = (unsigned short)f2bf(ev.w);
+            *(ushort4*)&u16p(dout, SCR_E16F)[((size_t)(b * NN + i)) * 512 + d4] = o;
+        } else {
+            const int jj = job - 2048;
+            const int b = jj >> 11, i = jj & 2047;
+            const int TI = i >> 7, li = i & 127;
+            const int tri = TI * (TI + 1) / 2;
+            const float linv = 1.f / dout[SCR_L + b * NN + i];
+            const unsigned short* WTb = w16pc(dout, b);
+            float* row = dout + OFF_QIJ + (size_t)b * 2 * NN * NN + (size_t)i * NN;
+            for (int j4 = t * 4; j4 < NN; j4 += 1024) {
+                const int tj = j4 >> 7;
+                float4 o = {0.f, 0.f, 0.f, 0.f};
+                if (tj <= TI) {
+                    ushort4 h = *(const ushort4*)&WTb[((size_t)(tri + tj)) * 16384
+                                                      + (size_t)li * 128 + (j4 & 127)];
+                    o.x = bf2f(h.x) * linv; o.y = bf2f(h.y) * linv;
+                    o.z = bf2f(h.z) * linv; o.w = bf2f(h.w) * linv;
+                }
+                *(float4*)&row[j4] = o;
+            }
+        }
+    }
+    gbar(dout);
+
+    {
+        const int job = blockIdx.x;
+        if (job < 256) {
+            const int z = job >> 7;
+            const int rem = job & 127;
+            const int d0 = (rem & 1) * 128;
+            const int by = rem >> 1;
+            const int b = by >> 4;
+            const int n0 = (by & 15) * 128;
+            const unsigned short* E16 = u16pc(dout, SCR_E16F) + (size_t)b * NN * 512;
+            const unsigned short* W16 = u16pc(dout, SCR_W16P) + (size_t)z * 131072;
+            const unsigned short* Abase = E16 + (size_t)n0 * 512;
+            const unsigned short* Bbase = W16 + (size_t)d0 * 512;
+
+            f32x4 acc[4][4];
+#pragma unroll
+            for (int i = 0; i < 4; ++i)
+#pragma unroll
+                for (int j = 0; j < 4; ++j) acc[i][j] = (f32x4){0.f, 0.f, 0.f, 0.f};
+
+            for (int kt = 0; kt < 16; ++kt) {
+                const int kk0 = kt * 32;
+                stage_tile(Abase + kk0, 512, Al, t);
+                stage_tile(Bbase + kk0, 512, Bl, t);
+                __syncthreads();
+                bf16x8 af[4], bff[4];
+#pragma unroll
+                for (int mi = 0; mi < 4; ++mi) af[mi] = *(const bf16x8*)&Al[(wm + mi * 16 + lm) * 32 + quad * 8];
+#pragma unroll
+                for (int nj = 0; nj < 4; ++nj) bff[nj] = *(const bf16x8*)&Bl[(wn + nj * 16 + lm) * 32 + quad * 8];
+#pragma unroll
+                for (int mi = 0; mi < 4; ++mi)
+#pragma unroll
+                    for (int nj = 0; nj < 4; ++nj)
+                        acc[mi][nj] = __builtin_amdgcn_mfma_f32_16x16x32_bf16(af[mi], bff[nj], acc[mi][nj], 0, 0, 0);
+                __syncthreads();
+            }
+            const int bofs = z ? DD : 0;
+            float* O = dout + OFF_OUT + (size_t)(b * 2 + z) * NN * DD;
+#pragma unroll
+            for (int mi = 0; mi < 4; ++mi)
+#pragma unroll
+                for (int r = 0; r < 4; ++r) {
+                    const int m = n0 + wm + mi * 16 + quad * 4 + r;
+#pragma unroll
+                    for (int nj = 0; nj < 4; ++nj) {
+                        const int d = d0 + wn + nj * 16 + lm;
+                        O[(size_t)m * DD + d] = acc[mi][nj][r] + bp[bofs + d];
+                    }
+                }
+        }
+    }
 }
 
 extern "C" void kernel_launch(void* const* d_in, const int* in_sizes, int n_in,
@@ -568,16 +581,13 @@
     const float* lamC = (const float*)d_in[17];
     float* out = (float*)d_out;
 
-    k_cvt<<<dim3(2048, 1, 5), dim3(256), 0, stream>>>(
-        Zq, Zk, Zv, Wq, Wk, Wv, Wp, tau, delta, lamOm, lamGa, lamC, out);
-    k_qkv<<<dim3(2, 64, 4), dim3(256), 0, stream>>>(bq, bk, bv, out);
-    k_vtrans<<<dim3(32, 4, 4), dim3(256), 0, stream>>>(out);
-    k_scores<<<dim3(136, 4), dim3(256), 0, stream>>>(tm, out);
-    k_estinner<<<dim3(60, 4), dim3(256), 0, stream>>>(out);
-    k_blendfills<<<dim3(2048, 1, 16), dim3(256), 0, stream>>>(out);
-    k_outproj<<<dim3(2, 64, 2), dim3(256), 0, stream>>>(bp, out);
+    hipMemsetAsync((void*)(out + SCR_SC + 8), 0, 8, stream);
+    k_mega<<<dim3(NBLK), dim3(256), 0, stream>>>(
+        Zq, Zk, Zv, tm, Wq, bq, Wk, bk, Wv, bv, Wp, bp,
+        lamOm, lamGa, tau, delta, lamC, out);
+
+    hipMemsetAsync((void*)(out + SCR_B0),    0, (size_t)NN * NN * 4, stream);
+    hipMemsetAsync((void*)(out + SCR_E16F),  0, (size_t)NN * NN * 4, stream);
     hipMemsetAsync((void*)(out + SCR_Z16F),  0, (size_t)NN * NN * 4, stream);
     hipMemsetAsync((void*)(out + SCR_Z16VF), 0, (size_t)NN * NN * 4, stream);
-    hipMemsetAsync((void*)(out + SCR_E16F),  0, (size_t)NN * NN * 4, stream);
-    hipMemsetAsync((void*)(out + SCR_QN),    0, ((size_t)NN * NN - 3145728) * 4, stream);
-}
+}
```
